# Performance work log

Hardware: AMD Instinct MI355X
Metric: run time of the kernel (lower is better)

Reference implementation:

```python
import jax, jax.numpy as jnp
import numpy as np

B, LATENT, HIDDEN, HEAD_H, OUT = 262144, 64, 512, 64, 4
EPS = 1e-5


def _layernorm(a, g, b):
    mu = jnp.mean(a, axis=-1, keepdims=True)
    var = jnp.mean(jnp.square(a - mu), axis=-1, keepdims=True)
    return (a - mu) / jnp.sqrt(var + EPS) * g + b


def _leaky(a):
    return jnp.where(a >= 0, a, 0.2 * a)


def setup_inputs() -> dict:
    key = jax.random.key(0)
    ks = jax.random.split(key, 12)
    s = lambda fan_in: 1.0 / np.sqrt(fan_in)
    return {
        "z": jax.random.normal(ks[0], (B, LATENT), dtype=jnp.float32),
        "x": jax.random.randint(ks[1], (B,), 0, 2, dtype=jnp.int32),
        "y": jax.random.randint(ks[2], (B,), 0, 2, dtype=jnp.int32),
        # encoder params (Linear stored as [in, out])
        "W1": jax.random.normal(ks[3], (LATENT, HIDDEN), dtype=jnp.float32) * s(LATENT),
        "b1": jnp.zeros((HIDDEN,), dtype=jnp.float32),
        "g1": jnp.ones((HIDDEN,), dtype=jnp.float32),
        "beta1": jnp.zeros((HIDDEN,), dtype=jnp.float32),
        "W2": jax.random.normal(ks[4], (HIDDEN, HIDDEN), dtype=jnp.float32) * s(HIDDEN),
        "b2": jnp.zeros((HIDDEN,), dtype=jnp.float32),
        "g2": jnp.ones((HIDDEN,), dtype=jnp.float32),
        "beta2": jnp.zeros((HIDDEN,), dtype=jnp.float32),
        # 4 setting-specific heads, stacked on leading axis k = 2*x + y
        "Wh1": jax.random.normal(ks[5], (4, HIDDEN, HEAD_H), dtype=jnp.float32) * s(HIDDEN),
        "bh1": jnp.zeros((4, HEAD_H), dtype=jnp.float32),
        "Wh2": jax.random.normal(ks[6], (4, HEAD_H, OUT), dtype=jnp.float32) * s(HEAD_H),
        "bh2": jnp.zeros((4, OUT), dtype=jnp.float32),
    }


def reference(z, x, y, W1, b1, g1, beta1, W2, b2, g2, beta2, Wh1, bh1, Wh2, bh2):
    # encoder: Linear -> LayerNorm -> LeakyReLU(0.2), twice
    h = _leaky(_layernorm(z @ W1 + b1, g1, beta1))          # [B, HIDDEN]
    h = _leaky(_layernorm(h @ W2 + b2, g2, beta2))          # [B, HIDDEN]
    # all 4 heads in one pass, then per-row select (equivalent to mask routing)
    t = jax.nn.relu(jnp.einsum("bh,khd->bkd", h, Wh1) + bh1)  # [B, 4, HEAD_H]
    logits_all = jnp.einsum("bkd,kdo->bko", t, Wh2) + bh2     # [B, 4, OUT]
    k = 2 * x + y                                              # head index per row
    logits = logits_all[jnp.arange(logits_all.shape[0]), k]    # [B, OUT]
    return jax.nn.softmax(logits, axis=-1)
```

## Files before the change

kernel.cpp:

```cpp
#include <hip/hip_runtime.h>

#define MT 64
#define MTM 4
#define TS 520
#define NROWS 262144
#define EPSV 1e-5f

typedef __attribute__((ext_vector_type(8))) short short8;
typedef __attribute__((ext_vector_type(4))) float floatx4;
typedef __attribute__((ext_vector_type(2))) float floatx2;
typedef __attribute__((ext_vector_type(4))) unsigned int uintx4;
typedef __attribute__((ext_vector_type(2))) unsigned int uintx2;

__device__ __forceinline__ unsigned short f2bf(float f) {
    unsigned u = __builtin_bit_cast(unsigned, f);
    u += 0x7fff + ((u >> 16) & 1);
    return (unsigned short)(u >> 16);
}
__device__ __forceinline__ float bf2f(short s) {
    unsigned u = ((unsigned)(unsigned short)s) << 16;
    return __builtin_bit_cast(float, u);
}
__device__ __forceinline__ unsigned cvtpk(float a, float b) {
    unsigned r;
    asm("v_cvt_pk_bf16_f32 %0, %1, %2" : "=v"(r) : "v"(a), "v"(b));
    return r;
}
__device__ __forceinline__ floatx2 pk_add(floatx2 a, floatx2 b) {
    floatx2 d; asm("v_pk_add_f32 %0, %1, %2" : "=v"(d) : "v"(a), "v"(b)); return d;
}
__device__ __forceinline__ floatx2 pk_mul(floatx2 a, floatx2 b) {
    floatx2 d; asm("v_pk_mul_f32 %0, %1, %2" : "=v"(d) : "v"(a), "v"(b)); return d;
}
__device__ __forceinline__ floatx2 pk_fma(floatx2 a, floatx2 b, floatx2 c) {
    floatx2 d; asm("v_pk_fma_f32 %0, %1, %2, %3" : "=v"(d) : "v"(a), "v"(b), "v"(c)); return d;
}
template<int C>
__device__ __forceinline__ float dpp_add(float v) {
    int t = __builtin_amdgcn_update_dpp(0, __builtin_bit_cast(int, v), C, 0xf, 0xf, true);
    return v + __builtin_bit_cast(float, t);
}
__device__ __forceinline__ float red16(float v) {
    v = dpp_add<0x111>(v);
    v = dpp_add<0x112>(v);
    v = dpp_add<0x114>(v);
    v = dpp_add<0x118>(v);
    return v;
}

__global__ void convert_weights(const float* __restrict__ W1, const float* __restrict__ W2,
                                const float* __restrict__ Wh1, short* __restrict__ ws) {
    int idx = blockIdx.x * 256 + threadIdx.x;
    if (idx < 32768) {
        int j = idx & 7, lane = (idx >> 3) & 63, c = idx >> 9;
        int ks = c & 1, nt = (c >> 1) & 7, w = c >> 4;
        int k = ks * 32 + (lane >> 4) * 8 + j;
        int n = w * 128 + nt * 16 + (lane & 15);
        ws[idx] = (short)f2bf(W1[k * 512 + n]);
    } else if (idx < 32768 + 262144) {
        int jdx = idx - 32768;
        int j = jdx & 7, lane = (jdx >> 3) & 63, c = jdx >> 9;
        int nt = c & 7, ks = (c >> 3) & 15, w = c >> 7;
        int kp = ks * 32 + (lane >> 4) * 8 + j;
        int k  = (kp & 0x180) + ((kp & 7) << 4) + ((kp >> 3) & 15);
        int n = w * 128 + nt * 16 + (lane & 15);
        ws[idx] = (short)f2bf(W2[k * 512 + n]);
    } else if (idx < 32768 + 262144 + 131072) {
        int jdx = idx - (32768 + 262144);
        int j = jdx & 7, lane = (jdx >> 3) & 63, c = jdx >> 9;
        int nt = c & 3, ks = (c >> 2) & 15, w = c >> 6;
        int kp = ks * 32 + (lane >> 4) * 8 + j;
        int k  = (kp & 0x180) + ((kp & 7) << 4) + ((kp >> 3) & 15);
        int col = w * 64 + nt * 16 + (lane & 15);
        int kk = col >> 6, d = col & 63;
        ws[idx] = (short)f2bf(Wh1[(kk * 512 + k) * 64 + d]);
    }
}

__global__ __launch_bounds__(256, 2) void fused_kernel(
    const float* __restrict__ z, const int* __restrict__ x, const int* __restrict__ y,
    const float* __restrict__ b1, const float* __restrict__ g1, const float* __restrict__ be1,
    const float* __restrict__ b2, const float* __restrict__ g2, const float* __restrict__ be2,
    const float* __restrict__ bh1, const float* __restrict__ Wh2, const float* __restrict__ bh2,
    const short* __restrict__ ws, float* __restrict__ out)
{
    __shared__ __align__(16) short tile[MT * TS];
    __shared__ float psum[4][MT];
    __shared__ float psq[4][MT];
    __shared__ float rmean[MT];
    __shared__ float rrstd[MT];

    int tid  = threadIdx.x;
    int wave = tid >> 6;
    int lane = tid & 63;
    int quad = lane >> 4;
    int l16  = lane & 15;
    int blk0 = blockIdx.x * MT;
    int nslab = wave * 128;

    const short* bbase1 = ws + wave * (16 * 512) + lane * 8;
    const short* bbase2 = ws + 32768 + wave * (16 * 8 * 512) + lane * 8;
    const short* bbase3 = ws + 32768 + 262144 + wave * (16 * 4 * 512) + lane * 8;

    floatx4 acc[MTM][8];

#pragma unroll
    for (int mt = 0; mt < MTM; mt++)
#pragma unroll
        for (int nt = 0; nt < 8; nt++) acc[mt][nt] = (floatx4){0.f, 0.f, 0.f, 0.f};

    __builtin_amdgcn_s_setprio(1);
#pragma unroll
    for (int ks = 0; ks < 2; ks++) {
        short8 afr[MTM];
#pragma unroll
        for (int mt = 0; mt < MTM; mt++) {
            int row = blk0 + mt * 16 + l16;
            const float* zp = z + row * 64 + ks * 32 + quad * 8;
            floatx4 f0 = *(const floatx4*)zp;
            floatx4 f1 = *(const floatx4*)(zp + 4);
            uintx4 up;
            up[0] = cvtpk(f0[0], f0[1]); up[1] = cvtpk(f0[2], f0[3]);
            up[2] = cvtpk(f1[0], f1[1]); up[3] = cvtpk(f1[2], f1[3]);
            afr[mt] = __builtin_bit_cast(short8, up);
        }
#pragma unroll
        for (int nt = 0; nt < 8; nt++) {
            short8 b = *(const short8*)(bbase1 + (nt * 2 + ks) * 512);
#pragma unroll
            for (int mt = 0; mt < MTM; mt++)
                acc[mt][nt] = __builtin_amdgcn_mfma_f32_16x16x32_bf16(afr[mt], b, acc[mt][nt], 0, 0, 0);
        }
    }
    __builtin_amdgcn_s_setprio(0);

    {
        floatx2 s2[MTM][2] = {}, q2[MTM][2] = {};
#pragma unroll
        for (int nt = 0; nt < 8; nt++) {
            float bv = b1[nslab + nt * 16 + l16];
            floatx2 bb = {bv, bv};
#pragma unroll
            for (int mt = 0; mt < MTM; mt++) {
                floatx2 v01 = {acc[mt][nt][0], acc[mt][nt][1]};
                floatx2 v23 = {acc[mt][nt][2], acc[mt][nt][3]};
                v01 = pk_add(v01, bb); v23 = pk_add(v23, bb);
                acc[mt][nt][0] = v01[0]; acc[mt][nt][1] = v01[1];
                acc[mt][nt][2] = v23[0]; acc[mt][nt][3] = v23[1];
                s2[mt][0] = pk_add(s2[mt][0], v01); q2[mt][0] = pk_fma(v01, v01, q2[mt][0]);
                s2[mt][1] = pk_add(s2[mt][1], v23); q2[mt][1] = pk_fma(v23, v23, q2[mt][1]);
            }
        }
#pragma unroll
        for (int mt = 0; mt < MTM; mt++)
#pragma unroll
            for (int pr = 0; pr < 2; pr++) {
                s2[mt][pr][0] = red16(s2[mt][pr][0]); s2[mt][pr][1] = red16(s2[mt][pr][1]);
                q2[mt][pr][0] = red16(q2[mt][pr][0]); q2[mt][pr][1] = red16(q2[mt][pr][1]);
            }
        if (l16 == 15) {
#pragma unroll
            for (int mt = 0; mt < MTM; mt++)
#pragma unroll
                for (int pr = 0; pr < 2; pr++) {
                    int row = mt * 16 + quad * 4 + pr * 2;
                    *(floatx2*)&psum[wave][row] = s2[mt][pr];
                    *(floatx2*)&psq[wave][row]  = q2[mt][pr];
                }
        }
    }
    __syncthreads();
    if (tid < MT) {
        float s = psum[0][tid] + psum[1][tid] + psum[2][tid] + psum[3][tid];
        float q = psq[0][tid] + psq[1][tid] + psq[2][tid] + psq[3][tid];
        float mean = s * (1.f / 512.f);
        float var  = q * (1.f / 512.f) - mean * mean;
        rmean[tid] = -mean;
        rrstd[tid] = rsqrtf(var + EPSV);
    }
    __syncthreads();
    {
        floatx2 nm[MTM][2], rs[MTM][2];
#pragma unroll
        for (int mt = 0; mt < MTM; mt++)
#pragma unroll
            for (int pr = 0; pr < 2; pr++) {
                int row = mt * 16 + quad * 4 + pr * 2;
                nm[mt][pr] = *(const floatx2*)&rmean[row];
                rs[mt][pr] = *(const floatx2*)&rrstd[row];
            }
        floatx2 ggA[8], bbA[8];
#pragma unroll
        for (int nt = 0; nt < 8; nt++) {
            int col = nslab + nt * 16 + l16;
            float g = g1[col], be = be1[col];
            ggA[nt] = (floatx2){g, g}; bbA[nt] = (floatx2){be, be};
        }
#pragma unroll
        for (int mt = 0; mt < MTM; mt++)
#pragma unroll
            for (int pr = 0; pr < 2; pr++) {
                float fa[8], fb[8];
#pragma unroll
                for (int nt = 0; nt < 8; nt++) {
                    floatx2 v = {acc[mt][nt][2 * pr], acc[mt][nt][2 * pr + 1]};
                    floatx2 t = pk_mul(pk_add(v, nm[mt][pr]), rs[mt][pr]);
                    floatx2 f = pk_fma(t, ggA[nt], bbA[nt]);
                    fa[nt] = fmaxf(f[0], 0.2f * f[0]);
                    fb[nt] = fmaxf(f[1], 0.2f * f[1]);
                }
                int row = mt * 16 + quad * 4 + pr * 2;
                uintx4 ua, ub;
                ua[0] = cvtpk(fa[0], fa[1]); ua[1] = cvtpk(fa[2], fa[3]);
                ua[2] = cvtpk(fa[4], fa[5]); ua[3] = cvtpk(fa[6], fa[7]);
                ub[0] = cvtpk(fb[0], fb[1]); ub[1] = cvtpk(fb[2], fb[3]);
                ub[2] = cvtpk(fb[4], fb[5]); ub[3] = cvtpk(fb[6], fb[7]);
                *(uintx4*)&tile[row * TS + nslab + l16 * 8]       = ua;
                *(uintx4*)&tile[(row + 1) * TS + nslab + l16 * 8] = ub;
            }
    }
    __syncthreads();

#pragma unroll
    for (int mt = 0; mt < MTM; mt++)
#pragma unroll
        for (int nt = 0; nt < 8; nt++) acc[mt][nt] = (floatx4){0.f, 0.f, 0.f, 0.f};

    __builtin_amdgcn_s_setprio(1);
    for (int ks = 0; ks < 16; ks++) {
        short8 afr[MTM];
#pragma unroll
        for (int mt = 0; mt < MTM; mt++)
            afr[mt] = *(const short8*)&tile[(mt * 16 + l16) * TS + ks * 32 + quad * 8];
#pragma unroll
        for (int nt = 0; nt < 8; nt++) {
            short8 b = *(const short8*)(bbase2 + (ks * 8 + nt) * 512);
#pragma unroll
            for (int mt = 0; mt < MTM; mt++)
                acc[mt][nt] = __builtin_amdgcn_mfma_f32_16x16x32_bf16(afr[mt], b, acc[mt][nt], 0, 0, 0);
        }
    }
    __builtin_amdgcn_s_setprio(0);
    {
        floatx2 s2[MTM][2] = {}, q2[MTM][2] = {};
#pragma unroll
        for (int nt = 0; nt < 8; nt++) {
            float bv = b2[nslab + nt * 16 + l16];
            floatx2 bb = {bv, bv};
#pragma unroll
            for (int mt = 0; mt < MTM; mt++) {
                floatx2 v01 = {acc[mt][nt][0], acc[mt][nt][1]};
                floatx2 v23 = {acc[mt][nt][2], acc[mt][nt][3]};
                v01 = pk_add(v01, bb); v23 = pk_add(v23, bb);
                acc[mt][nt][0] = v01[0]; acc[mt][nt][1] = v01[1];
                acc[mt][nt][2] = v23[0]; acc[mt][nt][3] = v23[1];
                s2[mt][0] = pk_add(s2[mt][0], v01); q2[mt][0] = pk_fma(v01, v01, q2[mt][0]);
                s2[mt][1] = pk_add(s2[mt][1], v23); q2[mt][1] = pk_fma(v23, v23, q2[mt][1]);
            }
        }
#pragma unroll
        for (int mt = 0; mt < MTM; mt++)
#pragma unroll
            for (int pr = 0; pr < 2; pr++) {
                s2[mt][pr][0] = red16(s2[mt][pr][0]); s2[mt][pr][1] = red16(s2[mt][pr][1]);
                q2[mt][pr][0] = red16(q2[mt][pr][0]); q2[mt][pr][1] = red16(q2[mt][pr][1]);
            }
        if (l16 == 15) {
#pragma unroll
            for (int mt = 0; mt < MTM; mt++)
#pragma unroll
                for (int pr = 0; pr < 2; pr++) {
                    int row = mt * 16 + quad * 4 + pr * 2;
                    *(floatx2*)&psum[wave][row] = s2[mt][pr];
                    *(floatx2*)&psq[wave][row]  = q2[mt][pr];
                }
        }
    }
    __syncthreads();
    if (tid < MT) {
        float s = psum[0][tid] + psum[1][tid] + psum[2][tid] + psum[3][tid];
        float q = psq[0][tid] + psq[1][tid] + psq[2][tid] + psq[3][tid];
        float mean = s * (1.f / 512.f);
        float var  = q * (1.f / 512.f) - mean * mean;
        rmean[tid] = -mean;
        rrstd[tid] = rsqrtf(var + EPSV);
    }
    __syncthreads();
    {
        floatx2 nm[MTM][2], rs[MTM][2];
#pragma unroll
        for (int mt = 0; mt < MTM; mt++)
#pragma unroll
            for (int pr = 0; pr < 2; pr++) {
                int row = mt * 16 + quad * 4 + pr * 2;
                nm[mt][pr] = *(const floatx2*)&rmean[row];
                rs[mt][pr] = *(const floatx2*)&rrstd[row];
            }
        floatx2 ggA[8], bbA[8];
#pragma unroll
        for (int nt = 0; nt < 8; nt++) {
            int col = nslab + nt * 16 + l16;
            float g = g2[col], be = be2[col];
            ggA[nt] = (floatx2){g, g}; bbA[nt] = (floatx2){be, be};
        }
#pragma unroll
        for (int mt = 0; mt < MTM; mt++)
#pragma unroll
            for (int pr = 0; pr < 2; pr++) {
                float fa[8], fb[8];
#pragma unroll
                for (int nt = 0; nt < 8; nt++) {
                    floatx2 v = {acc[mt][nt][2 * pr], acc[mt][nt][2 * pr + 1]};
                    floatx2 t = pk_mul(pk_add(v, nm[mt][pr]), rs[mt][pr]);
                    floatx2 f = pk_fma(t, ggA[nt], bbA[nt]);
                    fa[nt] = fmaxf(f[0], 0.2f * f[0]);
                    fb[nt] = fmaxf(f[1], 0.2f * f[1]);
                }
                int row = mt * 16 + quad * 4 + pr * 2;
                uintx4 ua, ub;
                ua[0] = cvtpk(fa[0], fa[1]); ua[1] = cvtpk(fa[2], fa[3]);
                ua[2] = cvtpk(fa[4], fa[5]); ua[3] = cvtpk(fa[6], fa[7]);
                ub[0] = cvtpk(fb[0], fb[1]); ub[1] = cvtpk(fb[2], fb[3]);
                ub[2] = cvtpk(fb[4], fb[5]); ub[3] = cvtpk(fb[6], fb[7]);
                *(uintx4*)&tile[row * TS + nslab + l16 * 8]       = ua;
                *(uintx4*)&tile[(row + 1) * TS + nslab + l16 * 8] = ub;
            }
    }
    __syncthreads();

#pragma unroll
    for (int mt = 0; mt < MTM; mt++)
#pragma unroll
        for (int nt = 0; nt < 4; nt++) acc[mt][nt] = (floatx4){0.f, 0.f, 0.f, 0.f};

    __builtin_amdgcn_s_setprio(1);
    for (int ks = 0; ks < 16; ks++) {
        short8 afr[MTM];
#pragma unroll
        for (int mt = 0; mt < MTM; mt++)
            afr[mt] = *(const short8*)&tile[(mt * 16 + l16) * TS + ks * 32 + quad * 8];
#pragma unroll
        for (int nt = 0; nt < 4; nt++) {
            short8 b = *(const short8*)(bbase3 + (ks * 4 + nt) * 512);
#pragma unroll
            for (int mt = 0; mt < MTM; mt++)
                acc[mt][nt] = __builtin_amdgcn_mfma_f32_16x16x32_bf16(afr[mt], b, acc[mt][nt], 0, 0, 0);
        }
    }
    __builtin_amdgcn_s_setprio(0);
    __syncthreads();
    {
        float bh1v[4];
#pragma unroll
        for (int nt = 0; nt < 4; nt++) bh1v[nt] = bh1[wave * 64 + nt * 16 + l16];
#pragma unroll
        for (int mt = 0; mt < MTM; mt++)
#pragma unroll
            for (int r2 = 0; r2 < 4; r2++) {
                int row = mt * 16 + quad * 4 + r2;
                float f[4];
#pragma unroll
                for (int nt = 0; nt < 4; nt++) {
                    float v = acc[mt][nt][r2] + bh1v[nt];
                    f[nt] = (v > 0.f) ? v : 0.f;
                }
                uintx2 up = {cvtpk(f[0], f[1]), cvtpk(f[2], f[3])};
                *(uintx2*)&tile[row * TS + wave * 64 + l16 * 4] = up;
            }
    }
    __syncthreads();

    {
        int r = tid >> 2, is = tid & 3;
        int grow = blk0 + r;
        int kk = 2 * x[grow] + y[grow];
        const short* tp = &tile[r * TS + kk * 64 + is * 16];
        short8 ta = *(const short8*)tp;
        short8 tb = *(const short8*)(tp + 8);
        const float* wp = Wh2 + kk * 256;
        float lg0 = 0.f, lg1 = 0.f, lg2 = 0.f, lg3 = 0.f;
#pragma unroll
        for (int e = 0; e < 8; e++) {
            int d0 = (e & 3) * 16 + 4 * is + (e >> 2);
            float t0 = bf2f(ta[e]);
            floatx4 w0 = *(const floatx4*)(wp + d0 * 4);
            float t1 = bf2f(tb[e]);
            floatx4 w1 = *(const floatx4*)(wp + (d0 + 2) * 4);
            lg0 += t0 * w0[0] + t1 * w1[0];
            lg1 += t0 * w0[1] + t1 * w1[1];
            lg2 += t0 * w0[2] + t1 * w1[2];
            lg3 += t0 * w0[3] + t1 * w1[3];
        }
#pragma unroll
        for (int off = 1; off < 4; off <<= 1) {
            lg0 += __shfl_xor(lg0, off, 64);
            lg1 += __shfl_xor(lg1, off, 64);
            lg2 += __shfl_xor(lg2, off, 64);
            lg3 += __shfl_xor(lg3, off, 64);
        }
        if (is == 0) {
            lg0 += bh2[kk * 4 + 0]; lg1 += bh2[kk * 4 + 1];
            lg2 += bh2[kk * 4 + 2]; lg3 += bh2[kk * 4 + 3];
            float m = fmaxf(fmaxf(lg0, lg1), fmaxf(lg2, lg3));
            float e0 = __expf(lg0 - m), e1 = __expf(lg1 - m);
            float e2 = __expf(lg2 - m), e3 = __expf(lg3 - m);
            float inv = 1.f / (e0 + e1 + e2 + e3);
            floatx4 o = {e0 * inv, e1 * inv, e2 * inv, e3 * inv};
            *(floatx4*)(out + grow * 4) = o;
        }
    }
}

extern "C" void kernel_launch(void* const* d_in, const int* in_sizes, int n_in,
                              void* d_out, int out_size, void* d_ws, size_t ws_size,
                              hipStream_t stream) {
    const float* z   = (const float*)d_in[0];
    const int*   x   = (const int*)d_in[1];
    const int*   y   = (const int*)d_in[2];
    const float* W1  = (const float*)d_in[3];
    const float* b1  = (const float*)d_in[4];
    const float* g1  = (const float*)d_in[5];
    const float* be1 = (const float*)d_in[6];
    const float* W2  = (const float*)d_in[7];
    const float* b2  = (const float*)d_in[8];
    const float* g2  = (const float*)d_in[9];
    const float* be2 = (const float*)d_in[10];
    const float* Wh1 = (const float*)d_in[11];
    const float* bh1 = (const float*)d_in[12];
    const float* Wh2 = (const float*)d_in[13];
    const float* bh2 = (const float*)d_in[14];
    short* ws = (short*)d_ws;
    float* out = (float*)d_out;

    hipLaunchKernelGGL(convert_weights, dim3(1664), dim3(256), 0, stream, W1, W2, Wh1, ws);
    hipLaunchKernelGGL(fused_kernel, dim3(NROWS / MT), dim3(256), 0, stream,
                       z, x, y, b1, g1, be1, b2, g2, be2, bh1, Wh2, bh2,
                       (const short*)ws, out);
}
```

Baseline: 364.0 us.

## Use 128-row blocks with 8 waves, each owning a 64-column slab

The row tile per block grows from 64 to 128 and the block from 4 to 8 waves. Each wave now owns a 64-column output slab instead of 128, and the bf16 weight pre-swizzle for W1, W2 and Wh1 is rewritten to match. Each weight fragment loaded from global memory now feeds 8 row tiles instead of 4, which cuts weight traffic per row. The cost is twice as many LDS A-fragment reads per MFMA and a doubled LDS tile (about 133 KB), which likely limits each CU to one block, so waves from a second block can no longer hide the barrier stalls.

```diff
diff --git a/kernel.cpp b/kernel.cpp
--- a/kernel.cpp
+++ b/kernel.cpp
@@ -1,15 +1,14 @@
 #include <hip/hip_runtime.h>
 
-#define MT 64
-#define MTM 4
+#define NROWS 262144
+#define MT 128
+#define NBLK (NROWS / MT)
 #define TS 520
-#define NROWS 262144
 #define EPSV 1e-5f
 
 typedef __attribute__((ext_vector_type(8))) short short8;
 typedef __attribute__((ext_vector_type(4))) float floatx4;
 typedef __attribute__((ext_vector_type(2))) float floatx2;
-typedef __attribute__((ext_vector_type(4))) unsigned int uintx4;
 typedef __attribute__((ext_vector_type(2))) unsigned int uintx2;
 
 __device__ __forceinline__ unsigned short f2bf(float f) {
@@ -51,33 +50,35 @@
 __global__ void convert_weights(const float* __restrict__ W1, const float* __restrict__ W2,
                                 const float* __restrict__ Wh1, short* __restrict__ ws) {
     int idx = blockIdx.x * 256 + threadIdx.x;
+    int j = idx & 7, lane = (idx >> 3) & 63;
+    int q = lane >> 4, l16 = lane & 15;
     if (idx < 32768) {
-        int j = idx & 7, lane = (idx >> 3) & 63, c = idx >> 9;
-        int ks = c & 1, nt = (c >> 1) & 7, w = c >> 4;
-        int k = ks * 32 + (lane >> 4) * 8 + j;
-        int n = w * 128 + nt * 16 + (lane & 15);
+        int c = idx >> 9;
+        int ntl = c & 3, ks = (c >> 2) & 1, wn = c >> 3;
+        int k = ks * 32 + q * 8 + j;
+        int n = wn * 64 + ntl * 16 + l16;
         ws[idx] = (short)f2bf(W1[k * 512 + n]);
-    } else if (idx < 32768 + 262144) {
-        int jdx = idx - 32768;
-        int j = jdx & 7, lane = (jdx >> 3) & 63, c = jdx >> 9;
-        int nt = c & 7, ks = (c >> 3) & 15, w = c >> 7;
-        int kp = ks * 32 + (lane >> 4) * 8 + j;
-        int k  = (kp & 0x180) + ((kp & 7) << 4) + ((kp >> 3) & 15);
-        int n = w * 128 + nt * 16 + (lane & 15);
+    } else if (idx < 294912) {
+        int c = (idx - 32768) >> 9;
+        int ntl = c & 3, ks = (c >> 2) & 15, wn = c >> 6;
+        int P = ks * 32 + q * 8 + j;
+        int p = P & 63;
+        int k = (P >> 6) * 64 + (p & 3) * 16 + (p >> 2);
+        int n = wn * 64 + ntl * 16 + l16;
         ws[idx] = (short)f2bf(W2[k * 512 + n]);
-    } else if (idx < 32768 + 262144 + 131072) {
-        int jdx = idx - (32768 + 262144);
-        int j = jdx & 7, lane = (jdx >> 3) & 63, c = jdx >> 9;
-        int nt = c & 3, ks = (c >> 2) & 15, w = c >> 6;
-        int kp = ks * 32 + (lane >> 4) * 8 + j;
-        int k  = (kp & 0x180) + ((kp & 7) << 4) + ((kp >> 3) & 15);
-        int col = w * 64 + nt * 16 + (lane & 15);
-        int kk = col >> 6, d = col & 63;
+    } else if (idx < 425984) {
+        int c = (idx - 294912) >> 9;
+        int ntl = c & 1, ks = (c >> 1) & 15, wn = c >> 5;
+        int P = ks * 32 + q * 8 + j;
+        int p = P & 63;
+        int k = (P >> 6) * 64 + (p & 3) * 16 + (p >> 2);
+        int kk = wn >> 1;
+        int d = (wn & 1) * 32 + ntl * 16 + l16;
         ws[idx] = (short)f2bf(Wh1[(kk * 512 + k) * 64 + d]);
     }
 }
 
-__global__ __launch_bounds__(256, 2) void fused_kernel(
+__global__ __launch_bounds__(512, 2) void fused_kernel(
     const float* __restrict__ z, const int* __restrict__ x, const int* __restrict__ y,
     const float* __restrict__ b1, const float* __restrict__ g1, const float* __restrict__ be1,
     const float* __restrict__ b2, const float* __restrict__ g2, const float* __restrict__ be2,
@@ -85,8 +86,8 @@
     const short* __restrict__ ws, float* __restrict__ out)
 {
     __shared__ __align__(16) short tile[MT * TS];
-    __shared__ float psum[4][MT];
-    __shared__ float psq[4][MT];
+    __shared__ float psum[8][MT];
+    __shared__ float psq[8][MT];
     __shared__ float rmean[MT];
     __shared__ float rrstd[MT];
 
@@ -95,84 +96,78 @@
     int lane = tid & 63;
     int quad = lane >> 4;
     int l16  = lane & 15;
-    int blk0 = blockIdx.x * MT;
-    int nslab = wave * 128;
-
-    const short* bbase1 = ws + wave * (16 * 512) + lane * 8;
-    const short* bbase2 = ws + 32768 + wave * (16 * 8 * 512) + lane * 8;
-    const short* bbase3 = ws + 32768 + 262144 + wave * (16 * 4 * 512) + lane * 8;
-
-    floatx4 acc[MTM][8];
-
-#pragma unroll
-    for (int mt = 0; mt < MTM; mt++)
-#pragma unroll
-        for (int nt = 0; nt < 8; nt++) acc[mt][nt] = (floatx4){0.f, 0.f, 0.f, 0.f};
+    int row0 = blockIdx.x * MT;
+
+    const short* bbase1 = ws + wave * (8 * 512) + lane * 8;
+    const short* bbase2 = ws + 32768 + wave * (64 * 512) + lane * 8;
+    const short* bbase3 = ws + 294912 + wave * (32 * 512) + lane * 8;
+
+    floatx4 acc[8][4];
+
+#pragma unroll
+    for (int mt = 0; mt < 8; mt++)
+#pragma unroll
+        for (int ntl = 0; ntl < 4; ntl++) acc[mt][ntl] = (floatx4){0.f, 0.f, 0.f, 0.f};
 
     __builtin_amdgcn_s_setprio(1);
 #pragma unroll
     for (int ks = 0; ks < 2; ks++) {
-        short8 afr[MTM];
-#pragma unroll
-        for (int mt = 0; mt < MTM; mt++) {
-            int row = blk0 + mt * 16 + l16;
-            const float* zp = z + row * 64 + ks * 32 + quad * 8;
+        short8 afr[8];
+#pragma unroll
+        for (int mt = 0; mt < 8; mt++) {
+            const float* zp = z + (row0 + mt * 16 + l16) * 64 + ks * 32 + quad * 8;
             floatx4 f0 = *(const floatx4*)zp;
             floatx4 f1 = *(const floatx4*)(zp + 4);
-            uintx4 up;
-            up[0] = cvtpk(f0[0], f0[1]); up[1] = cvtpk(f0[2], f0[3]);
-            up[2] = cvtpk(f1[0], f1[1]); up[3] = cvtpk(f1[2], f1[3]);
-            afr[mt] = __builtin_bit_cast(short8, up);
-        }
-#pragma unroll
-        for (int nt = 0; nt < 8; nt++) {
-            short8 b = *(const short8*)(bbase1 + (nt * 2 + ks) * 512);
-#pragma unroll
-            for (int mt = 0; mt < MTM; mt++)
-                acc[mt][nt] = __builtin_amdgcn_mfma_f32_16x16x32_bf16(afr[mt], b, acc[mt][nt], 0, 0, 0);
+            uintx2 lo = {cvtpk(f0[0], f0[1]), cvtpk(f0[2], f0[3])};
+            uintx2 hi = {cvtpk(f1[0], f1[1]), cvtpk(f1[2], f1[3])};
+            afr[mt] = __builtin_bit_cast(short8,
+                (__attribute__((ext_vector_type(4))) unsigned int){lo[0], lo[1], hi[0], hi[1]});
+        }
+#pragma unroll
+        for (int ntl = 0; ntl < 4; ntl++) {
+            short8 b = *(const short8*)(bbase1 + (ks * 4 + ntl) * 512);
+#pragma unroll
+            for (int mt = 0; mt < 8; mt++)
+                acc[mt][ntl] = __builtin_amdgcn_mfma_f32_16x16x32_bf16(afr[mt], b, acc[mt][ntl], 0, 0, 0);
         }
     }
     __builtin_amdgcn_s_setprio(0);
 
     {
-        floatx2 s2[MTM][2] = {}, q2[MTM][2] = {};
-#pragma unroll
-        for (int nt = 0; nt < 8; nt++) {
-            float bv = b1[nslab + nt * 16 + l16];
-            floatx2 bb = {bv, bv};
-#pragma unroll
-            for (int mt = 0; mt < MTM; mt++) {
-                floatx2 v01 = {acc[mt][nt][0], acc[mt][nt][1]};
-                floatx2 v23 = {acc[mt][nt][2], acc[mt][nt][3]};
-                v01 = pk_add(v01, bb); v23 = pk_add(v23, bb);
-                acc[mt][nt][0] = v01[0]; acc[mt][nt][1] = v01[1];
-                acc[mt][nt][2] = v23[0]; acc[mt][nt][3] = v23[1];
-                s2[mt][0] = pk_add(s2[mt][0], v01); q2[mt][0] = pk_fma(v01, v01, q2[mt][0]);
-                s2[mt][1] = pk_add(s2[mt][1], v23); q2[mt][1] = pk_fma(v23, v23, q2[mt][1]);
-            }
-        }
-#pragma unroll
-        for (int mt = 0; mt < MTM; mt++)
-#pragma unroll
-            for (int pr = 0; pr < 2; pr++) {
-                s2[mt][pr][0] = red16(s2[mt][pr][0]); s2[mt][pr][1] = red16(s2[mt][pr][1]);
-                q2[mt][pr][0] = red16(q2[mt][pr][0]); q2[mt][pr][1] = red16(q2[mt][pr][1]);
-            }
-        if (l16 == 15) {
-#pragma unroll
-            for (int mt = 0; mt < MTM; mt++)
-#pragma unroll
-                for (int pr = 0; pr < 2; pr++) {
-                    int row = mt * 16 + quad * 4 + pr * 2;
-                    *(floatx2*)&psum[wave][row] = s2[mt][pr];
-                    *(floatx2*)&psq[wave][row]  = q2[mt][pr];
-                }
+        float bv[4];
+#pragma unroll
+        for (int ntl = 0; ntl < 4; ntl++) bv[ntl] = b1[wave * 64 + ntl * 16 + l16];
+#pragma unroll
+        for (int mt = 0; mt < 8; mt++) {
+            floatx2 s01 = {0.f, 0.f}, s23 = {0.f, 0.f}, q01 = {0.f, 0.f}, q23 = {0.f, 0.f};
+#pragma unroll
+            for (int ntl = 0; ntl < 4; ntl++) {
+                floatx2 bb = {bv[ntl], bv[ntl]};
+                floatx2 v01 = pk_add((floatx2){acc[mt][ntl][0], acc[mt][ntl][1]}, bb);
+                floatx2 v23 = pk_add((floatx2){acc[mt][ntl][2], acc[mt][ntl][3]}, bb);
+                acc[mt][ntl][0] = v01[0]; acc[mt][ntl][1] = v01[1];
+                acc[mt][ntl][2] = v23[0]; acc[mt][ntl][3] = v23[1];
+                s01 = pk_add(s01, v01); q01 = pk_fma(v01, v01, q01);
+                s23 = pk_add(s23, v23); q23 = pk_fma(v23, v23, q23);
+            }
+            s01[0] = red16(s01[0]); s01[1] = red16(s01[1]);
+            s23[0] = red16(s23[0]); s23[1] = red16(s23[1]);
+            q01[0] = red16(q01[0]); q01[1] = red16(q01[1]);
+            q23[0] = red16(q23[0]); q23[1] = red16(q23[1]);
+            if (l16 == 15) {
+                int row = mt * 16 + quad * 4;
+                *(floatx2*)&psum[wave][row]     = s01;
+                *(floatx2*)&psum[wave][row + 2] = s23;
+                *(floatx2*)&psq[wave][row]      = q01;
+                *(floatx2*)&psq[wave][row + 2]  = q23;
+            }
         }
     }
     __syncthreads();
     if (tid < MT) {
-        float s = psum[0][tid] + psum[1][tid] + psum[2][tid] + psum[3][tid];
-        float q = psq[0][tid] + psq[1][tid] + psq[2][tid] + psq[3][tid];
+        float s = 0.f, q = 0.f;
+#pragma unroll
+        for (int w = 0; w < 8; w++) { s += psum[w][tid]; q += psq[w][tid]; }
         float mean = s * (1.f / 512.f);
         float var  = q * (1.f / 512.f) - mean * mean;
         rmean[tid] = -mean;
@@ -180,106 +175,95 @@
     }
     __syncthreads();
     {
-        floatx2 nm[MTM][2], rs[MTM][2];
-#pragma unroll
-        for (int mt = 0; mt < MTM; mt++)
-#pragma unroll
-            for (int pr = 0; pr < 2; pr++) {
-                int row = mt * 16 + quad * 4 + pr * 2;
-                nm[mt][pr] = *(const floatx2*)&rmean[row];
-                rs[mt][pr] = *(const floatx2*)&rrstd[row];
-            }
-        floatx2 ggA[8], bbA[8];
-#pragma unroll
-        for (int nt = 0; nt < 8; nt++) {
-            int col = nslab + nt * 16 + l16;
-            float g = g1[col], be = be1[col];
-            ggA[nt] = (floatx2){g, g}; bbA[nt] = (floatx2){be, be};
-        }
-#pragma unroll
-        for (int mt = 0; mt < MTM; mt++)
-#pragma unroll
-            for (int pr = 0; pr < 2; pr++) {
-                float fa[8], fb[8];
-#pragma unroll
-                for (int nt = 0; nt < 8; nt++) {
-                    floatx2 v = {acc[mt][nt][2 * pr], acc[mt][nt][2 * pr + 1]};
-                    floatx2 t = pk_mul(pk_add(v, nm[mt][pr]), rs[mt][pr]);
-                    floatx2 f = pk_fma(t, ggA[nt], bbA[nt]);
-                    fa[nt] = fmaxf(f[0], 0.2f * f[0]);
-                    fb[nt] = fmaxf(f[1], 0.2f * f[1]);
-                }
-                int row = mt * 16 + quad * 4 + pr * 2;
-                uintx4 ua, ub;
-                ua[0] = cvtpk(fa[0], fa[1]); ua[1] = cvtpk(fa[2], fa[3]);
-                ua[2] = cvtpk(fa[4], fa[5]); ua[3] = cvtpk(fa[6], fa[7]);
-                ub[0] = cvtpk(fb[0], fb[1]); ub[1] = cvtpk(fb[2], fb[3]);
-                ub[2] = cvtpk(fb[4], fb[5]); ub[3] = cvtpk(fb[6], fb[7]);
-                *(uintx4*)&tile[row * TS + nslab + l16 * 8]       = ua;
-                *(uintx4*)&tile[(row + 1) * TS + nslab + l16 * 8] = ub;
-            }
-    }
-    __syncthreads();
-
-#pragma unroll
-    for (int mt = 0; mt < MTM; mt++)
-#pragma unroll
-        for (int nt = 0; nt < 8; nt++) acc[mt][nt] = (floatx4){0.f, 0.f, 0.f, 0.f};
+        float gv[4], bev[4];
+#pragma unroll
+        for (int ntl = 0; ntl < 4; ntl++) {
+            int col = wave * 64 + ntl * 16 + l16;
+            gv[ntl] = g1[col]; bev[ntl] = be1[col];
+        }
+#pragma unroll
+        for (int mt = 0; mt < 8; mt++) {
+            int rb = mt * 16 + quad * 4;
+            floatx2 nm01 = *(const floatx2*)&rmean[rb];
+            floatx2 nm23 = *(const floatx2*)&rmean[rb + 2];
+            floatx2 rs01 = *(const floatx2*)&rrstd[rb];
+            floatx2 rs23 = *(const floatx2*)&rrstd[rb + 2];
+            float fv[4][4];
+#pragma unroll
+            for (int ntl = 0; ntl < 4; ntl++) {
+                floatx2 gg = {gv[ntl], gv[ntl]}, bb = {bev[ntl], bev[ntl]};
+                floatx2 t01 = pk_fma(pk_mul(pk_add((floatx2){acc[mt][ntl][0], acc[mt][ntl][1]}, nm01), rs01), gg, bb);
+                floatx2 t23 = pk_fma(pk_mul(pk_add((floatx2){acc[mt][ntl][2], acc[mt][ntl][3]}, nm23), rs23), gg, bb);
+                fv[ntl][0] = fmaxf(t01[0], 0.2f * t01[0]);
+                fv[ntl][1] = fmaxf(t01[1], 0.2f * t01[1]);
+                fv[ntl][2] = fmaxf(t23[0], 0.2f * t23[0]);
+                fv[ntl][3] = fmaxf(t23[1], 0.2f * t23[1]);
+            }
+#pragma unroll
+            for (int r2 = 0; r2 < 4; r2++) {
+                uintx2 up = {cvtpk(fv[0][r2], fv[1][r2]), cvtpk(fv[2][r2], fv[3][r2])};
+                *(uintx2*)&tile[(rb + r2) * TS + wave * 64 + l16 * 4] = up;
+            }
+        }
+    }
+    __syncthreads();
+
+#pragma unroll
+    for (int mt = 0; mt < 8; mt++)
+#pragma unroll
+        for (int ntl = 0; ntl < 4; ntl++) acc[mt][ntl] = (floatx4){0.f, 0.f, 0.f, 0.f};
 
     __builtin_amdgcn_s_setprio(1);
     for (int ks = 0; ks < 16; ks++) {
-        short8 afr[MTM];
-#pragma unroll
-        for (int mt = 0; mt < MTM; mt++)
+        short8 afr[8];
+#pragma unroll
+        for (int mt = 0; mt < 8; mt++)
             afr[mt] = *(const short8*)&tile[(mt * 16 + l16) * TS + ks * 32 + quad * 8];
 #pragma unroll
-        for (int nt = 0; nt < 8; nt++) {
-            short8 b = *(const short8*)(bbase2 + (ks * 8 + nt) * 512);
-#pragma unroll
-            for (int mt = 0; mt < MTM; mt++)
-                acc[mt][nt] = __builtin_amdgcn_mfma_f32_16x16x32_bf16(afr[mt], b, acc[mt][nt], 0, 0, 0);
+        for (int ntl = 0; ntl < 4; ntl++) {
+            short8 b = *(const short8*)(bbase2 + (ks * 4 + ntl) * 512);
+#pragma unroll
+            for (int mt = 0; mt < 8; mt++)
+                acc[mt][ntl] = __builtin_amdgcn_mfma_f32_16x16x32_bf16(afr[mt], b, acc[mt][ntl], 0, 0, 0);
         }
     }
     __builtin_amdgcn_s_setprio(0);
-    {
-        floatx2 s2[MTM][2] = {}, q2[MTM][2] = {};
-#pragma unroll
-        for (int nt = 0; nt < 8; nt++) {
-            float bv = b2[nslab + nt * 16 + l16];
-            floatx2 bb = {bv, bv};
-#pragma unroll
-            for (int mt = 0; mt < MTM; mt++) {
-                floatx2 v01 = {acc[mt][nt][0], acc[mt][nt][1]};
-                floatx2 v23 = {acc[mt][nt][2], acc[mt][nt][3]};
-                v01 = pk_add(v01, bb); v23 = pk_add(v23, bb);
-                acc[mt][nt][0] = v01[0]; acc[mt][nt][1] = v01[1];
-                acc[mt][nt][2] = v23[0]; acc[mt][nt][3] = v23[1];
-                s2[mt][0] = pk_add(s2[mt][0], v01); q2[mt][0] = pk_fma(v01, v01, q2[mt][0]);
-                s2[mt][1] = pk_add(s2[mt][1], v23); q2[mt][1] = pk_fma(v23, v23, q2[mt][1]);
-            }
-        }
-#pragma unroll
-        for (int mt = 0; mt < MTM; mt++)
-#pragma unroll
-            for (int pr = 0; pr < 2; pr++) {
-                s2[mt][pr][0] = red16(s2[mt][pr][0]); s2[mt][pr][1] = red16(s2[mt][pr][1]);
-                q2[mt][pr][0] = red16(q2[mt][pr][0]); q2[mt][pr][1] = red16(q2[mt][pr][1]);
-            }
-        if (l16 == 15) {
-#pragma unroll
-            for (int mt = 0; mt < MTM; mt++)
-#pragma unroll
-                for (int pr = 0; pr < 2; pr++) {
-                    int row = mt * 16 + quad * 4 + pr * 2;
-                    *(floatx2*)&psum[wave][row] = s2[mt][pr];
-                    *(floatx2*)&psq[wave][row]  = q2[mt][pr];
-                }
+
+    {
+        float bv[4];
+#pragma unroll
+        for (int ntl = 0; ntl < 4; ntl++) bv[ntl] = b2[wave * 64 + ntl * 16 + l16];
+#pragma unroll
+        for (int mt = 0; mt < 8; mt++) {
+            floatx2 s01 = {0.f, 0.f}, s23 = {0.f, 0.f}, q01 = {0.f, 0.f}, q23 = {0.f, 0.f};
+#pragma unroll
+            for (int ntl = 0; ntl < 4; ntl++) {
+                floatx2 bb = {bv[ntl], bv[ntl]};
+                floatx2 v01 = pk_add((floatx2){acc[mt][ntl][0], acc[mt][ntl][1]}, bb);
+                floatx2 v23 = pk_add((floatx2){acc[mt][ntl][2], acc[mt][ntl][3]}, bb);
+                acc[mt][ntl][0] = v01[0]; acc[mt][ntl][1] = v01[1];
+                acc[mt][ntl][2] = v23[0]; acc[mt][ntl][3] = v23[1];
+                s01 = pk_add(s01, v01); q01 = pk_fma(v01, v01, q01);
+                s23 = pk_add(s23, v23); q23 = pk_fma(v23, v23, q23);
+            }
+            s01[0] = red16(s01[0]); s01[1] = red16(s01[1]);
+            s23[0] = red16(s23[0]); s23[1] = red16(s23[1]);
+            q01[0] = red16(q01[0]); q01[1] = red16(q01[1]);
+            q23[0] = red16(q23[0]); q23[1] = red16(q23[1]);
+            if (l16 == 15) {
+                int row = mt * 16 + quad * 4;
+                *(floatx2*)&psum[wave][row]     = s01;
+                *(floatx2*)&psum[wave][row + 2] = s23;
+                *(floatx2*)&psq[wave][row]      = q01;
+                *(floatx2*)&psq[wave][row + 2]  = q23;
+            }
         }
     }
     __syncthreads();
     if (tid < MT) {
-        float s = psum[0][tid] + psum[1][tid] + psum[2][tid] + psum[3][tid];
-        float q = psq[0][tid] + psq[1][tid] + psq[2][tid] + psq[3][tid];
+        float s = 0.f, q = 0.f;
+#pragma unroll
+        for (int w = 0; w < 8; w++) { s += psum[w][tid]; q += psq[w][tid]; }
         float mean = s * (1.f / 512.f);
         float var  = q * (1.f / 512.f) - mean * mean;
         rmean[tid] = -mean;
@@ -287,92 +271,82 @@
     }
     __syncthreads();
     {
-        floatx2 nm[MTM][2], rs[MTM][2];
-#pragma unroll
-        for (int mt = 0; mt < MTM; mt++)
-#pragma unroll
-            for (int pr = 0; pr < 2; pr++) {
-                int row = mt * 16 + quad * 4 + pr * 2;
-                nm[mt][pr] = *(const floatx2*)&rmean[row];
-                rs[mt][pr] = *(const floatx2*)&rrstd[row];
-            }
-        floatx2 ggA[8], bbA[8];
-#pragma unroll
-        for (int nt = 0; nt < 8; nt++) {
-            int col = nslab + nt * 16 + l16;
-            float g = g2[col], be = be2[col];
-            ggA[nt] = (floatx2){g, g}; bbA[nt] = (floatx2){be, be};
-        }
-#pragma unroll
-        for (int mt = 0; mt < MTM; mt++)
-#pragma unroll
-            for (int pr = 0; pr < 2; pr++) {
-                float fa[8], fb[8];
-#pragma unroll
-                for (int nt = 0; nt < 8; nt++) {
-                    floatx2 v = {acc[mt][nt][2 * pr], acc[mt][nt][2 * pr + 1]};
-                    floatx2 t = pk_mul(pk_add(v, nm[mt][pr]), rs[mt][pr]);
-                    floatx2 f = pk_fma(t, ggA[nt], bbA[nt]);
-                    fa[nt] = fmaxf(f[0], 0.2f * f[0]);
-                    fb[nt] = fmaxf(f[1], 0.2f * f[1]);
-                }
-                int row = mt * 16 + quad * 4 + pr * 2;
-                uintx4 ua, ub;
-                ua[0] = cvtpk(fa[0], fa[1]); ua[1] = cvtpk(fa[2], fa[3]);
-                ua[2] = cvtpk(fa[4], fa[5]); ua[3] = cvtpk(fa[6], fa[7]);
-                ub[0] = cvtpk(fb[0], fb[1]); ub[1] = cvtpk(fb[2], fb[3]);
-                ub[2] = cvtpk(fb[4], fb[5]); ub[3] = cvtpk(fb[6], fb[7]);
-                *(uintx4*)&tile[row * TS + nslab + l16 * 8]       = ua;
-                *(uintx4*)&tile[(row + 1) * TS + nslab + l16 * 8] = ub;
-            }
-    }
-    __syncthreads();
-
-#pragma unroll
-    for (int mt = 0; mt < MTM; mt++)
-#pragma unroll
-        for (int nt = 0; nt < 4; nt++) acc[mt][nt] = (floatx4){0.f, 0.f, 0.f, 0.f};
+        float gv[4], bev[4];
+#pragma unroll
+        for (int ntl = 0; ntl < 4; ntl++) {
+            int col = wave * 64 + ntl * 16 + l16;
+            gv[ntl] = g2[col]; bev[ntl] = be2[col];
+        }
+#pragma unroll
+        for (int mt = 0; mt < 8; mt++) {
+            int rb = mt * 16 + quad * 4;
+            floatx2 nm01 = *(const floatx2*)&rmean[rb];
+            floatx2 nm23 = *(const floatx2*)&rmean[rb + 2];
+            floatx2 rs01 = *(const floatx2*)&rrstd[rb];
+            floatx2 rs23 = *(const floatx2*)&rrstd[rb + 2];
+            float fv[4][4];
+#pragma unroll
+            for (int ntl = 0; ntl < 4; ntl++) {
+                floatx2 gg = {gv[ntl], gv[ntl]}, bb = {bev[ntl], bev[ntl]};
+                floatx2 t01 = pk_fma(pk_mul(pk_add((floatx2){acc[mt][ntl][0], acc[mt][ntl][1]}, nm01), rs01), gg, bb);
+                floatx2 t23 = pk_fma(pk_mul(pk_add((floatx2){acc[mt][ntl][2], acc[mt][ntl][3]}, nm23), rs23), gg, bb);
+                fv[ntl][0] = fmaxf(t01[0], 0.2f * t01[0]);
+                fv[ntl][1] = fmaxf(t01[1], 0.2f * t01[1]);
+                fv[ntl][2] = fmaxf(t23[0], 0.2f * t23[0]);
+                fv[ntl][3] = fmaxf(t23[1], 0.2f * t23[1]);
+            }
+#pragma unroll
+            for (int r2 = 0; r2 < 4; r2++) {
+                uintx2 up = {cvtpk(fv[0][r2], fv[1][r2]), cvtpk(fv[2][r2], fv[3][r2])};
+                *(uintx2*)&tile[(rb + r2) * TS + wave * 64 + l16 * 4] = up;
+            }
+        }
+    }
+    __syncthreads();
+
+#pragma unroll
+    for (int mt = 0; mt < 8; mt++)
+#pragma unroll
+        for (int ntl = 0; ntl < 2; ntl++) acc[mt][ntl] = (floatx4){0.f, 0.f, 0.f, 0.f};
 
     __builtin_amdgcn_s_setprio(1);
     for (int ks = 0; ks < 16; ks++) {
-        short8 afr[MTM];
-#pragma unroll
-        for (int mt = 0; mt < MTM; mt++)
+        short8 afr[8];
+#pragma unroll
+        for (int mt = 0; mt < 8; mt++)
             afr[mt] = *(const short8*)&tile[(mt * 16 + l16) * TS + ks * 32 + quad * 8];
 #pragma unroll
-        for (int nt = 0; nt < 4; nt++) {
-            short8 b = *(const short8*)(bbase3 + (ks * 4 + nt) * 512);
-#pragma unroll
-            for (int mt = 0; mt < MTM; mt++)
-                acc[mt][nt] = __builtin_amdgcn_mfma_f32_16x16x32_bf16(afr[mt], b, acc[mt][nt], 0, 0, 0);
+        for (int ntl = 0; ntl < 2; ntl++) {
+            short8 b = *(const short8*)(bbase3 + (ks * 2 + ntl) * 512);
+#pragma unroll
+            for (int mt = 0; mt < 8; mt++)
+                acc[mt][ntl] = __builtin_amdgcn_mfma_f32_16x16x32_bf16(afr[mt], b, acc[mt][ntl], 0, 0, 0);
         }
     }
     __builtin_amdgcn_s_setprio(0);
     __syncthreads();
-    {
-        float bh1v[4];
-#pragma unroll
-        for (int nt = 0; nt < 4; nt++) bh1v[nt] = bh1[wave * 64 + nt * 16 + l16];
-#pragma unroll
-        for (int mt = 0; mt < MTM; mt++)
+
+    {
+        float bh1v[2];
+#pragma unroll
+        for (int ntl = 0; ntl < 2; ntl++) bh1v[ntl] = bh1[wave * 32 + ntl * 16 + l16];
+#pragma unroll
+        for (int mt = 0; mt < 8; mt++)
 #pragma unroll
             for (int r2 = 0; r2 < 4; r2++) {
                 int row = mt * 16 + quad * 4 + r2;
-                float f[4];
-#pragma unroll
-                for (int nt = 0; nt < 4; nt++) {
-                    float v = acc[mt][nt][r2] + bh1v[nt];
-                    f[nt] = (v > 0.f) ? v : 0.f;
-                }
-                uintx2 up = {cvtpk(f[0], f[1]), cvtpk(f[2], f[3])};
-                *(uintx2*)&tile[row * TS + wave * 64 + l16 * 4] = up;
+                float f0 = acc[mt][0][r2] + bh1v[0];
+                float f1 = acc[mt][1][r2] + bh1v[1];
+                f0 = (f0 > 0.f) ? f0 : 0.f;
+                f1 = (f1 > 0.f) ? f1 : 0.f;
+                *(unsigned int*)&tile[row * TS + wave * 32 + l16 * 2] = cvtpk(f0, f1);
             }
     }
     __syncthreads();
 
     {
         int r = tid >> 2, is = tid & 3;
-        int grow = blk0 + r;
+        int grow = row0 + r;
         int kk = 2 * x[grow] + y[grow];
         const short* tp = &tile[r * TS + kk * 64 + is * 16];
         short8 ta = *(const short8*)tp;
@@ -381,15 +355,21 @@
         float lg0 = 0.f, lg1 = 0.f, lg2 = 0.f, lg3 = 0.f;
 #pragma unroll
         for (int e = 0; e < 8; e++) {
-            int d0 = (e & 3) * 16 + 4 * is + (e >> 2);
+            int u = is * 16 + e;
+            int d = (u >> 5) * 32 + (u & 1) * 16 + ((u >> 1) & 15);
             float t0 = bf2f(ta[e]);
-            floatx4 w0 = *(const floatx4*)(wp + d0 * 4);
+            floatx4 w0 = *(const floatx4*)(wp + d * 4);
+            lg0 += t0 * w0[0]; lg1 += t0 * w0[1];
+            lg2 += t0 * w0[2]; lg3 += t0 * w0[3];
+        }
+#pragma unroll
+        for (int e = 0; e < 8; e++) {
+            int u = is * 16 + 8 + e;
+            int d = (u >> 5) * 32 + (u & 1) * 16 + ((u >> 1) & 15);
             float t1 = bf2f(tb[e]);
-            floatx4 w1 = *(const floatx4*)(wp + (d0 + 2) * 4);
-            lg0 += t0 * w0[0] + t1 * w1[0];
-            lg1 += t0 * w0[1] + t1 * w1[1];
-            lg2 += t0 * w0[2] + t1 * w1[2];
-            lg3 += t0 * w0[3] + t1 * w1[3];
+            floatx4 w1 = *(const floatx4*)(wp + d * 4);
+            lg0 += t1 * w1[0]; lg1 += t1 * w1[1];
+            lg2 += t1 * w1[2]; lg3 += t1 * w1[3];
         }
 #pragma unroll
         for (int off = 1; off < 4; off <<= 1) {
@@ -433,7 +413,7 @@
     float* out = (float*)d_out;
 
     hipLaunchKernelGGL(convert_weights, dim3(1664), dim3(256), 0, stream, W1, W2, Wh1, ws);
-    hipLaunchKernelGGL(fused_kernel, dim3(NROWS / MT), dim3(256), 0, stream,
+    hipLaunchKernelGGL(fused_kernel, dim3(NBLK), dim3(512), 0, stream,
                        z, x, y, b1, g1, be1, b2, g2, be2, bh1, Wh2, bh2,
                        (const short*)ws, out);
 }
```

New measurement: 435.0 us. 19.5% more time.
